# Optimization experiments

Hardware: AMD Instinct MI355X
Metric: run time of the kernel (lower is better)

## Reference

```python
import jax, jax.numpy as jnp
import numpy as np

N, C, F = 2048, 512, 512

def setup_inputs() -> dict:
    key = jax.random.key(0)
    k1, k2 = jax.random.split(key)
    x = jax.random.normal(k1, (N, F), dtype=jnp.float32)
    means = jax.random.normal(k2, (C, F), dtype=jnp.float32)
    return {"x": x, "means": means}

def reference(x, means):
    # Negative squared Euclidean distance from each sample to each class mean.
    # diff: (N, C, F) broadcasted; output: (N, C)
    diff = x[:, None, :] - means[None, :, :]
    return -jnp.sum(diff * diff, axis=-1)
```

## Files before the change

### kernel.cpp

```cpp
#include <hip/hip_runtime.h>
#include <hip/hip_bf16.h>
#include <string.h>


#define F_DIM  512
#define C_ROWS 512

typedef __attribute__((ext_vector_type(8))) short short8;
typedef __attribute__((ext_vector_type(4))) float f32x4;

static __device__ __forceinline__ unsigned pk_bf16(float lo, float hi) {
    __hip_bfloat162 h = __float22bfloat162_rn(make_float2(lo, hi));
    unsigned u;
    memcpy(&u, &h, 4);
    return u;
}

__global__ __launch_bounds__(1024) void ncm_fused(
        const float* __restrict__ x, const float* __restrict__ means,
        float* __restrict__ out) {
    __shared__ __align__(16) short As[64 * 512];
    __shared__ __align__(16) short Bs[64 * 512];
    __shared__ float xn_s[64], mn_s[64];

    const int d  = blockIdx.x;
    const int by = (d & 7) * 4 + ((d >> 3) & 3);
    const int bx = d >> 5;
    const int rowBase = by * 64, colBase = bx * 64;

    const int t    = threadIdx.x;
    const int w    = t >> 6;
    const int lane = t & 63;
    const int qr   = lane >> 4;
    const int ql   = lane & 15;

    {
        const int half  = w >> 3;
        const int wrow8 = (w & 7) * 8;
        const float* src = (half == 0) ? x + (size_t)rowBase * F_DIM
                                       : means + (size_t)colBase * F_DIM;
        short* dst = (half == 0) ? As : Bs;
        float* nrm = (half == 0) ? xn_s : mn_s;

#pragma unroll
        for (int i = 0; i < 2; i++) {
            const int r = wrow8 + i * 4 + qr;
            const float* rowp = src + (size_t)r * F_DIM;
            float4 va[4][2];
#pragma unroll
            for (int ph = 0; ph < 4; ph++) {
                const float* p = rowp + ph * 128 + ql * 8;
                va[ph][0] = *(const float4*)p;
                va[ph][1] = *(const float4*)(p + 4);
            }
            float ss = 0.f;
#pragma unroll
            for (int ph = 0; ph < 4; ph++) {
                float vv[8] = {va[ph][0].x, va[ph][0].y, va[ph][0].z, va[ph][0].w,
                               va[ph][1].x, va[ph][1].y, va[ph][1].z, va[ph][1].w};
#pragma unroll
                for (int j = 0; j < 8; j++) ss += vv[j] * vv[j];
                int4 o;
                o.x = (int)pk_bf16(vv[0], vv[1]);
                o.y = (int)pk_bf16(vv[2], vv[3]);
                o.z = (int)pk_bf16(vv[4], vv[5]);
                o.w = (int)pk_bf16(vv[6], vv[7]);
                const int slot = ph * 16 + ql;
                *(int4*)(dst + r * F_DIM + ((slot ^ (r & 7)) << 3)) = o;
            }
            ss += __shfl_xor(ss, 1);
            ss += __shfl_xor(ss, 2);
            ss += __shfl_xor(ss, 4);
            ss += __shfl_xor(ss, 8);
            if (ql == 0) nrm[r] = ss;
        }
    }
    __syncthreads();

    const int quad = w & 3;
    const int kh   = w >> 2;
    const int wr   = (quad >> 1) * 32;
    const int wc   = (quad & 1) * 32;

    f32x4 acc[2][2];
#pragma unroll
    for (int mi = 0; mi < 2; mi++)
#pragma unroll
        for (int ni = 0; ni < 2; ni++)
            acc[mi][ni] = (f32x4){0.f, 0.f, 0.f, 0.f};

#pragma unroll
    for (int j = 0; j < 4; j++) {
        const int kk   = kh * 4 + j;
        const int slot = kk * 4 + (lane >> 4);
        short8 a[2], b[2];
#pragma unroll
        for (int mi = 0; mi < 2; mi++) {
            const int r = wr + mi * 16 + (lane & 15);
            a[mi] = *(const short8*)(As + r * F_DIM + ((slot ^ (r & 7)) << 3));
        }
#pragma unroll
        for (int ni = 0; ni < 2; ni++) {
            const int r = wc + ni * 16 + (lane & 15);
            b[ni] = *(const short8*)(Bs + r * F_DIM + ((slot ^ (r & 7)) << 3));
        }
#pragma unroll
        for (int mi = 0; mi < 2; mi++)
#pragma unroll
            for (int ni = 0; ni < 2; ni++)
                acc[mi][ni] = __builtin_amdgcn_mfma_f32_16x16x32_bf16(
                    a[mi], b[ni], acc[mi][ni], 0, 0, 0);
    }

    __syncthreads();
    float* red = (float*)As;
    if (kh > 0) {
        const int g = kh - 1;
        float* base = red + (g * 4 + quad) * 1024 + lane * 16;
#pragma unroll
        for (int s = 0; s < 4; s++) {
            const int sw = s ^ ((lane >> 1) & 3);
            *(f32x4*)(base + sw * 4) = acc[s >> 1][s & 1];
        }
    }
    __syncthreads();
    if (kh == 0) {
#pragma unroll
        for (int g = 0; g < 3; g++) {
            const float* base = red + (g * 4 + quad) * 1024 + lane * 16;
#pragma unroll
            for (int s = 0; s < 4; s++) {
                const int sw = s ^ ((lane >> 1) & 3);
                f32x4 v = *(const f32x4*)(base + sw * 4);
#pragma unroll
                for (int j = 0; j < 4; j++) acc[s >> 1][s & 1][j] += v[j];
            }
        }

        float xn[2][4];
#pragma unroll
        for (int mi = 0; mi < 2; mi++)
#pragma unroll
            for (int j = 0; j < 4; j++)
                xn[mi][j] = xn_s[wr + mi * 16 + (lane >> 4) * 4 + j];

#pragma unroll
        for (int ni = 0; ni < 2; ni++) {
            const int cl = wc + ni * 16 + (lane & 15);
            const int c  = colBase + cl;
            const float mn = mn_s[cl];
#pragma unroll
            for (int mi = 0; mi < 2; mi++) {
                const int rbase = rowBase + wr + mi * 16 + (lane >> 4) * 4;
#pragma unroll
                for (int j = 0; j < 4; j++)
                    out[(size_t)(rbase + j) * C_ROWS + c] =
                        2.0f * acc[mi][ni][j] - xn[mi][j] - mn;
            }
        }
    }
}

extern "C" void kernel_launch(void* const* d_in, const int* in_sizes, int n_in,
                              void* d_out, int out_size, void* d_ws, size_t ws_size,
                              hipStream_t stream) {
    const float* x     = (const float*)d_in[0];
    const float* means = (const float*)d_in[1];
    float* out = (float*)d_out;
    ncm_fused<<<256, 1024, 0, stream>>>(x, means, out);
}
```

Baseline: 11.62 us.

## Double-buffer K chunks to overlap global loads with MFMA compute

Splits the K dimension into four 128-wide chunks staged through a double-buffered LDS tile, so the next chunk's global loads are issued while MFMAs run on the current one. LDS drops from two full 64x512 tiles to four 64x128 tiles, and the norm accumulation and conversion are spread across the chunk loop. The cost is three extra block-wide barriers and fewer global loads in flight per thread at any one time, which can reduce memory-level parallelism in a kernel that is mostly load-bound.

```diff
diff --git a/kernel.cpp b/kernel.cpp
--- a/kernel.cpp
+++ b/kernel.cpp
@@ -5,6 +5,7 @@
 
 #define F_DIM  512
 #define C_ROWS 512
+#define BK     128
 
 typedef __attribute__((ext_vector_type(8))) short short8;
 typedef __attribute__((ext_vector_type(4))) float f32x4;
@@ -19,8 +20,7 @@
 __global__ __launch_bounds__(1024) void ncm_fused(
         const float* __restrict__ x, const float* __restrict__ means,
         float* __restrict__ out) {
-    __shared__ __align__(16) short As[64 * 512];
-    __shared__ __align__(16) short Bs[64 * 512];
+    __shared__ __align__(16) short lds[2][2][64 * BK];
     __shared__ float xn_s[64], mn_s[64];
 
     const int d  = blockIdx.x;
@@ -31,50 +31,40 @@
     const int t    = threadIdx.x;
     const int w    = t >> 6;
     const int lane = t & 63;
-    const int qr   = lane >> 4;
-    const int ql   = lane & 15;
+    const int sr   = t >> 4;
+    const int sslt = t & 15;
+    const int skey = sr & 15;
 
-    {
-        const int half  = w >> 3;
-        const int wrow8 = (w & 7) * 8;
-        const float* src = (half == 0) ? x + (size_t)rowBase * F_DIM
-                                       : means + (size_t)colBase * F_DIM;
-        short* dst = (half == 0) ? As : Bs;
-        float* nrm = (half == 0) ? xn_s : mn_s;
+    const float* xrow = x + (size_t)(rowBase + sr) * F_DIM + sslt * 8;
+    const float* mrow = means + (size_t)(colBase + sr) * F_DIM + sslt * 8;
+    short* ldsA0 = &lds[0][0][sr * BK + ((sslt ^ skey) << 3)];
+    short* ldsB0 = &lds[0][1][sr * BK + ((sslt ^ skey) << 3)];
+    short* ldsA1 = &lds[1][0][sr * BK + ((sslt ^ skey) << 3)];
+    short* ldsB1 = &lds[1][1][sr * BK + ((sslt ^ skey) << 3)];
 
-#pragma unroll
-        for (int i = 0; i < 2; i++) {
-            const int r = wrow8 + i * 4 + qr;
-            const float* rowp = src + (size_t)r * F_DIM;
-            float4 va[4][2];
-#pragma unroll
-            for (int ph = 0; ph < 4; ph++) {
-                const float* p = rowp + ph * 128 + ql * 8;
-                va[ph][0] = *(const float4*)p;
-                va[ph][1] = *(const float4*)(p + 4);
-            }
-            float ss = 0.f;
-#pragma unroll
-            for (int ph = 0; ph < 4; ph++) {
-                float vv[8] = {va[ph][0].x, va[ph][0].y, va[ph][0].z, va[ph][0].w,
-                               va[ph][1].x, va[ph][1].y, va[ph][1].z, va[ph][1].w};
-#pragma unroll
-                for (int j = 0; j < 8; j++) ss += vv[j] * vv[j];
-                int4 o;
-                o.x = (int)pk_bf16(vv[0], vv[1]);
-                o.y = (int)pk_bf16(vv[2], vv[3]);
-                o.z = (int)pk_bf16(vv[4], vv[5]);
-                o.w = (int)pk_bf16(vv[6], vv[7]);
-                const int slot = ph * 16 + ql;
-                *(int4*)(dst + r * F_DIM + ((slot ^ (r & 7)) << 3)) = o;
-            }
-            ss += __shfl_xor(ss, 1);
-            ss += __shfl_xor(ss, 2);
-            ss += __shfl_xor(ss, 4);
-            ss += __shfl_xor(ss, 8);
-            if (ql == 0) nrm[r] = ss;
-        }
-    }
+    float ssA = 0.f, ssB = 0.f;
+    float4 ra0, ra1, rb0, rb1;
+
+#define CVT_WRITE(pA, pB)                                                    \
+    do {                                                                     \
+        float va[8] = {ra0.x, ra0.y, ra0.z, ra0.w, ra1.x, ra1.y, ra1.z, ra1.w}; \
+        float vb[8] = {rb0.x, rb0.y, rb0.z, rb0.w, rb1.x, rb1.y, rb1.z, rb1.w}; \
+        int4 oA, oB;                                                         \
+        oA.x = (int)pk_bf16(va[0], va[1]); oA.y = (int)pk_bf16(va[2], va[3]); \
+        oA.z = (int)pk_bf16(va[4], va[5]); oA.w = (int)pk_bf16(va[6], va[7]); \
+        oB.x = (int)pk_bf16(vb[0], vb[1]); oB.y = (int)pk_bf16(vb[2], vb[3]); \
+        oB.z = (int)pk_bf16(vb[4], vb[5]); oB.w = (int)pk_bf16(vb[6], vb[7]); \
+        _Pragma("unroll")                                                    \
+        for (int j = 0; j < 8; j++) { ssA += va[j] * va[j]; ssB += vb[j] * vb[j]; } \
+        *(int4*)(pA) = oA;                                                   \
+        *(int4*)(pB) = oB;                                                   \
+    } while (0)
+
+    ra0 = *(const float4*)(xrow);
+    ra1 = *(const float4*)(xrow + 4);
+    rb0 = *(const float4*)(mrow);
+    rb1 = *(const float4*)(mrow + 4);
+    CVT_WRITE(ldsA0, ldsB0);
     __syncthreads();
 
     const int quad = w & 3;
@@ -90,30 +80,48 @@
             acc[mi][ni] = (f32x4){0.f, 0.f, 0.f, 0.f};
 
 #pragma unroll
-    for (int j = 0; j < 4; j++) {
-        const int kk   = kh * 4 + j;
-        const int slot = kk * 4 + (lane >> 4);
-        short8 a[2], b[2];
+    for (int k = 0; k < 4; k++) {
+        if (k < 3) {
+            ra0 = *(const float4*)(xrow + (k + 1) * BK);
+            ra1 = *(const float4*)(xrow + (k + 1) * BK + 4);
+            rb0 = *(const float4*)(mrow + (k + 1) * BK);
+            rb1 = *(const float4*)(mrow + (k + 1) * BK + 4);
+        }
+        {
+            const short* A = lds[k & 1][0];
+            const short* B = lds[k & 1][1];
+            const int slot = kh * 4 + (lane >> 4);
+            short8 a[2], b[2];
 #pragma unroll
-        for (int mi = 0; mi < 2; mi++) {
-            const int r = wr + mi * 16 + (lane & 15);
-            a[mi] = *(const short8*)(As + r * F_DIM + ((slot ^ (r & 7)) << 3));
+            for (int mi = 0; mi < 2; mi++) {
+                const int r = wr + mi * 16 + (lane & 15);
+                a[mi] = *(const short8*)(A + r * BK + ((slot ^ (r & 15)) << 3));
+            }
+#pragma unroll
+            for (int ni = 0; ni < 2; ni++) {
+                const int r = wc + ni * 16 + (lane & 15);
+                b[ni] = *(const short8*)(B + r * BK + ((slot ^ (r & 15)) << 3));
+            }
+#pragma unroll
+            for (int mi = 0; mi < 2; mi++)
+#pragma unroll
+                for (int ni = 0; ni < 2; ni++)
+                    acc[mi][ni] = __builtin_amdgcn_mfma_f32_16x16x32_bf16(
+                        a[mi], b[ni], acc[mi][ni], 0, 0, 0);
         }
-#pragma unroll
-        for (int ni = 0; ni < 2; ni++) {
-            const int r = wc + ni * 16 + (lane & 15);
-            b[ni] = *(const short8*)(Bs + r * F_DIM + ((slot ^ (r & 7)) << 3));
-        }
-#pragma unroll
-        for (int mi = 0; mi < 2; mi++)
-#pragma unroll
-            for (int ni = 0; ni < 2; ni++)
-                acc[mi][ni] = __builtin_amdgcn_mfma_f32_16x16x32_bf16(
-                    a[mi], b[ni], acc[mi][ni], 0, 0, 0);
+        if (k == 0) CVT_WRITE(ldsA1, ldsB1);
+        else if (k == 1) CVT_WRITE(ldsA0, ldsB0);
+        else if (k == 2) CVT_WRITE(ldsA1, ldsB1);
+        __syncthreads();
     }
 
-    __syncthreads();
-    float* red = (float*)As;
+    ssA += __shfl_xor(ssA, 1);  ssB += __shfl_xor(ssB, 1);
+    ssA += __shfl_xor(ssA, 2);  ssB += __shfl_xor(ssB, 2);
+    ssA += __shfl_xor(ssA, 4);  ssB += __shfl_xor(ssB, 4);
+    ssA += __shfl_xor(ssA, 8);  ssB += __shfl_xor(ssB, 8);
+    if (sslt == 0) { xn_s[sr] = ssA; mn_s[sr] = ssB; }
+
+    float* red = (float*)lds;
     if (kh > 0) {
         const int g = kh - 1;
         float* base = red + (g * 4 + quad) * 1024 + lane * 16;
@@ -159,6 +167,7 @@
             }
         }
     }
+#undef CVT_WRITE
 }
 
 extern "C" void kernel_launch(void* const* d_in, const int* in_sizes, int n_in,
```

Result: no change. 11.61 us (-0.1%).
